# Kernel tuning notes

Hardware: AMD Instinct MI355X
Metric: run time of the kernel (lower is better)

The kernel has to match this reference:

```python
import jax, jax.numpy as jnp
import numpy as np


def _idft_matrix(n):
    # IDFT_n[j,k] = (1/n) * exp(+2*pi*i*j*k/n)  (matches 1/N * DFT**(-1) in source)
    jk = np.outer(np.arange(n), np.arange(n))
    return jnp.asarray((np.exp(2j * np.pi * jk / n) / n).astype(np.complex64))


def setup_inputs() -> dict:
    key = jax.random.key(0)
    B, Y, X = 64, 512, 512
    inp = jax.random.normal(key, (B, Y, X, 2), dtype=jnp.float32)
    return {"inp": inp}


def reference(inp) -> jnp.ndarray:
    B, Y, X, _ = inp.shape
    # pack real/imag channels into complex64
    c = jax.lax.complex(inp[..., 0], inp[..., 1])  # [B, Y, X]
    IDFT_y = _idft_matrix(Y)  # [Y, Y]
    IDFT_x = _idft_matrix(X)  # [X, X]
    # IDFT along Y axis: 'db,abc->adc'
    res1 = jnp.einsum('db,abc->adc', IDFT_y, c)
    # IDFT along X axis then magnitude: 'cd,abc->abd'
    out = jnp.abs(jnp.einsum('cd,abc->abd', IDFT_x, res1))
    return out[..., None]  # [B, Y, X, 1]
```

## Files before the change

kernel.cpp:

```cpp
#include <hip/hip_runtime.h>
#include <math.h>


#define TWO_PI_F 6.283185307179586f

__device__ __forceinline__ float2 cmul(float2 a, float2 b) {
    return make_float2(a.x * b.x - a.y * b.y, a.x * b.y + a.y * b.x);
}
__device__ __forceinline__ float2 cadd(float2 a, float2 b) { return make_float2(a.x + b.x, a.y + b.y); }
__device__ __forceinline__ float2 csub(float2 a, float2 b) { return make_float2(a.x - b.x, a.y - b.y); }
__device__ __forceinline__ float2 csq(float2 a) { return make_float2(a.x * a.x - a.y * a.y, 2.f * a.x * a.y); }
__device__ __forceinline__ unsigned rev9(unsigned v) { return __brev(v) >> 23; }
__device__ __forceinline__ unsigned rev6(unsigned v) { return __brev(v) >> 26; }

__device__ __forceinline__ void fft512(float2* r, float2 A, int l) {
    const float S = 0.70710678118654752f;
    {
        float2 t0 = A;
        float2 t1 = cmul(A, make_float2(S, S));
        float2 t2 = make_float2(-A.y, A.x);
        float2 t3 = cmul(A, make_float2(-S, S));
        float2 u, v;
        u = r[0]; v = r[4]; r[0] = cadd(u, v); r[4] = cmul(csub(u, v), t0);
        u = r[1]; v = r[5]; r[1] = cadd(u, v); r[5] = cmul(csub(u, v), t1);
        u = r[2]; v = r[6]; r[2] = cadd(u, v); r[6] = cmul(csub(u, v), t2);
        u = r[3]; v = r[7]; r[3] = cadd(u, v); r[7] = cmul(csub(u, v), t3);
    }
    float2 A2 = csq(A);
    {
        float2 A2i = make_float2(-A2.y, A2.x);
        float2 u, v;
        u = r[0]; v = r[2]; r[0] = cadd(u, v); r[2] = cmul(csub(u, v), A2);
        u = r[1]; v = r[3]; r[1] = cadd(u, v); r[3] = cmul(csub(u, v), A2i);
        u = r[4]; v = r[6]; r[4] = cadd(u, v); r[6] = cmul(csub(u, v), A2);
        u = r[5]; v = r[7]; r[5] = cadd(u, v); r[7] = cmul(csub(u, v), A2i);
    }
    float2 A4 = csq(A2);
    {
        float2 u, v;
        u = r[0]; v = r[1]; r[0] = cadd(u, v); r[1] = cmul(csub(u, v), A4);
        u = r[2]; v = r[3]; r[2] = cadd(u, v); r[3] = cmul(csub(u, v), A4);
        u = r[4]; v = r[5]; r[4] = cadd(u, v); r[5] = cmul(csub(u, v), A4);
        u = r[6]; v = r[7]; r[6] = cadd(u, v); r[7] = cmul(csub(u, v), A4);
    }
    float2 P = csq(A4);
    #pragma unroll
    for (int mi = 0; mi < 6; ++mi) {
        const int m = 32 >> mi;
        const bool hi = (l & m) != 0;
        #pragma unroll
        for (int k = 0; k < 8; ++k) {
            float2 o;
            o.x = __shfl_xor(r[k].x, m);
            o.y = __shfl_xor(r[k].y, m);
            float2 sum = cadd(r[k], o);
            float2 dif = cmul(csub(r[k], o), P);
            r[k].x = hi ? dif.x : sum.x;
            r[k].y = hi ? dif.y : sum.y;
        }
        if (mi < 5) P = csq(P);
    }
}

__global__ __launch_bounds__(512)
void fft_y_kernel(const float2* __restrict__ in, float2* __restrict__ ws) {
    __shared__ float2 tile[4096];
    const int t = threadIdx.x;
    const int w = t >> 6, l = t & 63;
    const int g = t & 7, q = t >> 3;
    const int x0 = blockIdx.x * 8;
    const int b = blockIdx.y;

    const float2* src = in + ((size_t)b << 18) + x0;
    const int sw = (q & 7) ^ ((q >> 3) & 7);
    #pragma unroll
    for (int it = 0; it < 8; ++it) {
        const int y = it * 64 + q;
        tile[y * 8 + (g ^ sw)] = src[((size_t)y << 9) + g];
    }
    __syncthreads();

    float sA, cA;
    sincosf(TWO_PI_F * (float)l * (1.0f / 512.0f), &sA, &cA);
    float2 r[8];
    const int swl = (l & 7) ^ ((l >> 3) & 7);
    #pragma unroll
    for (int k = 0; k < 8; ++k)
        r[k] = tile[(k * 64 + l) * 8 + (w ^ swl)];

    fft512(r, make_float2(cA, sA), l);

    #pragma unroll
    for (int k = 0; k < 8; ++k)
        tile[(k * 64 + l) * 8 + (w ^ swl)] = r[k];
    __syncthreads();

    float2* dst = ws + ((size_t)b << 18) + x0;
    #pragma unroll
    for (int it = 0; it < 8; ++it) {
        const int y = it * 64 + q;
        dst[((size_t)y << 9) + g] = tile[y * 8 + (g ^ sw)];
    }
}

__global__ __launch_bounds__(256)
void fft_x_mag_kernel(const float2* __restrict__ ws, float* __restrict__ out) {
    const int t = threadIdx.x;
    const int w = t >> 6, l = t & 63;
    const int row = blockIdx.x * 4 + w;
    const int b = row >> 9, ry = row & 511;

    const float2* src = ws + ((size_t)row << 9);
    float2 r[8];
    #pragma unroll
    for (int k = 0; k < 8; ++k)
        r[k] = src[k * 64 + l];

    float sA, cA;
    sincosf(TWO_PI_F * (float)l * (1.0f / 512.0f), &sA, &cA);
    fft512(r, make_float2(cA, sA), l);

    const int rev3k[8] = {0, 4, 2, 6, 1, 5, 3, 7};
    float m[8];
    #pragma unroll
    for (int k = 0; k < 8; ++k) {
        const float2 z = r[k];
        m[rev3k[k]] = sqrtf(z.x * z.x + z.y * z.y) * (1.0f / 262144.0f);
    }

    float* orow = out + (((size_t)(b << 9) + rev9(ry)) << 9);
    const int base = rev6(l) * 8;
    *(float4*)(orow + base)     = make_float4(m[0], m[1], m[2], m[3]);
    *(float4*)(orow + base + 4) = make_float4(m[4], m[5], m[6], m[7]);
}

extern "C" void kernel_launch(void* const* d_in, const int* in_sizes, int n_in,
                              void* d_out, int out_size, void* d_ws, size_t ws_size,
                              hipStream_t stream) {
    const float2* in = (const float2*)d_in[0];
    float2* ws = (float2*)d_ws;
    float* out = (float*)d_out;

    fft_y_kernel<<<dim3(64, 64), 512, 0, stream>>>(in, ws);
    fft_x_mag_kernel<<<8192, 256, 0, stream>>>(ws, out);
}
```

Measured before the change: 294.6 us.

## Store Y-FFT output transposed in natural order; X-FFT reads columns via shared tile

The Y-pass kernel now writes its result directly from registers into a transposed workspace layout ([b][x][y]) with bit-reversal undone per thread. This removes the second shared-memory round trip and the extra barrier. The X-pass kernel switches to tiled loads of 8 columns through swizzled shared memory with float4 global reads, so its output rows come out in natural order and the rev9 row scatter goes away. Global loads are widened to float4 in both kernels. In exchange, both passes now depend on strided-column gathers, and the workspace writes are scattered at 32-byte granularity, which may hurt coalescing.

Result: slower. 303.1 us (+2.9%).

```diff
diff --git a/kernel.cpp b/kernel.cpp
--- a/kernel.cpp
+++ b/kernel.cpp
@@ -10,7 +10,6 @@
 __device__ __forceinline__ float2 cadd(float2 a, float2 b) { return make_float2(a.x + b.x, a.y + b.y); }
 __device__ __forceinline__ float2 csub(float2 a, float2 b) { return make_float2(a.x - b.x, a.y - b.y); }
 __device__ __forceinline__ float2 csq(float2 a) { return make_float2(a.x * a.x - a.y * a.y, 2.f * a.x * a.y); }
-__device__ __forceinline__ unsigned rev9(unsigned v) { return __brev(v) >> 23; }
 __device__ __forceinline__ unsigned rev6(unsigned v) { return __brev(v) >> 26; }
 
 __device__ __forceinline__ void fft512(float2* r, float2 A, int l) {
@@ -63,84 +62,94 @@
 }
 
 __global__ __launch_bounds__(512)
-void fft_y_kernel(const float2* __restrict__ in, float2* __restrict__ ws) {
-    __shared__ float2 tile[4096];
+void fft_y_kernel(const float2* __restrict__ in, float2* __restrict__ wst) {
+    __shared__ float2 tile[8 * 512];
     const int t = threadIdx.x;
     const int w = t >> 6, l = t & 63;
-    const int g = t & 7, q = t >> 3;
+    const int g = t & 3, q = t >> 2;
     const int x0 = blockIdx.x * 8;
-    const int b = blockIdx.y;
+    const int b  = blockIdx.y;
 
     const float2* src = in + ((size_t)b << 18) + x0;
-    const int sw = (q & 7) ^ ((q >> 3) & 7);
     #pragma unroll
-    for (int it = 0; it < 8; ++it) {
-        const int y = it * 64 + q;
-        tile[y * 8 + (g ^ sw)] = src[((size_t)y << 9) + g];
+    for (int it = 0; it < 4; ++it) {
+        const int y = it * 128 + q;
+        const float4 v = *(const float4*)(src + ((size_t)y << 9) + 2 * g);
+        const int ys = y ^ (4 * g);
+        tile[(2 * g) * 512 + ys]     = make_float2(v.x, v.y);
+        tile[(2 * g + 1) * 512 + ys] = make_float2(v.z, v.w);
     }
     __syncthreads();
 
     float sA, cA;
     sincosf(TWO_PI_F * (float)l * (1.0f / 512.0f), &sA, &cA);
     float2 r[8];
-    const int swl = (l & 7) ^ ((l >> 3) & 7);
+    const int sw = 4 * (w >> 1);
     #pragma unroll
     for (int k = 0; k < 8; ++k)
-        r[k] = tile[(k * 64 + l) * 8 + (w ^ swl)];
+        r[k] = tile[w * 512 + ((k * 64 + l) ^ sw)];
 
     fft512(r, make_float2(cA, sA), l);
 
-    #pragma unroll
-    for (int k = 0; k < 8; ++k)
-        tile[(k * 64 + l) * 8 + (w ^ swl)] = r[k];
-    __syncthreads();
-
-    float2* dst = ws + ((size_t)b << 18) + x0;
-    #pragma unroll
-    for (int it = 0; it < 8; ++it) {
-        const int y = it * 64 + q;
-        dst[((size_t)y << 9) + g] = tile[y * 8 + (g ^ sw)];
-    }
+    float2* dst = wst + (((size_t)(b * 512 + x0 + w)) << 9) + rev6((unsigned)l) * 8;
+    *(float4*)(dst + 0) = make_float4(r[0].x, r[0].y, r[4].x, r[4].y);
+    *(float4*)(dst + 2) = make_float4(r[2].x, r[2].y, r[6].x, r[6].y);
+    *(float4*)(dst + 4) = make_float4(r[1].x, r[1].y, r[5].x, r[5].y);
+    *(float4*)(dst + 6) = make_float4(r[3].x, r[3].y, r[7].x, r[7].y);
 }
 
-__global__ __launch_bounds__(256)
-void fft_x_mag_kernel(const float2* __restrict__ ws, float* __restrict__ out) {
+__global__ __launch_bounds__(512)
+void fft_x_mag_kernel(const float2* __restrict__ wst, float* __restrict__ out) {
+    __shared__ float2 tile[8 * 512];
     const int t = threadIdx.x;
     const int w = t >> 6, l = t & 63;
-    const int row = blockIdx.x * 4 + w;
-    const int b = row >> 9, ry = row & 511;
+    const int g = t & 3, q = t >> 2;
+    const int f0 = blockIdx.x * 8;
+    const int b  = blockIdx.y;
 
-    const float2* src = ws + ((size_t)row << 9);
-    float2 r[8];
+    const float2* src = wst + ((size_t)b << 18) + f0;
     #pragma unroll
-    for (int k = 0; k < 8; ++k)
-        r[k] = src[k * 64 + l];
+    for (int it = 0; it < 4; ++it) {
+        const int x = it * 128 + q;
+        const float4 v = *(const float4*)(src + ((size_t)x << 9) + 2 * g);
+        const int xs = x ^ (4 * g);
+        tile[(2 * g) * 512 + xs]     = make_float2(v.x, v.y);
+        tile[(2 * g + 1) * 512 + xs] = make_float2(v.z, v.w);
+    }
+    __syncthreads();
 
     float sA, cA;
     sincosf(TWO_PI_F * (float)l * (1.0f / 512.0f), &sA, &cA);
+    float2 r[8];
+    const int sw = 4 * (w >> 1);
+    #pragma unroll
+    for (int k = 0; k < 8; ++k)
+        r[k] = tile[w * 512 + ((k * 64 + l) ^ sw)];
+
     fft512(r, make_float2(cA, sA), l);
 
-    const int rev3k[8] = {0, 4, 2, 6, 1, 5, 3, 7};
-    float m[8];
-    #pragma unroll
-    for (int k = 0; k < 8; ++k) {
-        const float2 z = r[k];
-        m[rev3k[k]] = sqrtf(z.x * z.x + z.y * z.y) * (1.0f / 262144.0f);
-    }
+    const float s = 1.0f / 262144.0f;
+    float m0 = sqrtf(r[0].x * r[0].x + r[0].y * r[0].y) * s;
+    float m1 = sqrtf(r[4].x * r[4].x + r[4].y * r[4].y) * s;
+    float m2 = sqrtf(r[2].x * r[2].x + r[2].y * r[2].y) * s;
+    float m3 = sqrtf(r[6].x * r[6].x + r[6].y * r[6].y) * s;
+    float m4 = sqrtf(r[1].x * r[1].x + r[1].y * r[1].y) * s;
+    float m5 = sqrtf(r[5].x * r[5].x + r[5].y * r[5].y) * s;
+    float m6 = sqrtf(r[3].x * r[3].x + r[3].y * r[3].y) * s;
+    float m7 = sqrtf(r[7].x * r[7].x + r[7].y * r[7].y) * s;
 
-    float* orow = out + (((size_t)(b << 9) + rev9(ry)) << 9);
-    const int base = rev6(l) * 8;
-    *(float4*)(orow + base)     = make_float4(m[0], m[1], m[2], m[3]);
-    *(float4*)(orow + base + 4) = make_float4(m[4], m[5], m[6], m[7]);
+    float* orow = out + (((size_t)(b * 512 + f0 + w)) << 9) + rev6((unsigned)l) * 8;
+    *(float4*)(orow + 0) = make_float4(m0, m1, m2, m3);
+    *(float4*)(orow + 4) = make_float4(m4, m5, m6, m7);
 }
 
 extern "C" void kernel_launch(void* const* d_in, const int* in_sizes, int n_in,
                               void* d_out, int out_size, void* d_ws, size_t ws_size,
                               hipStream_t stream) {
     const float2* in = (const float2*)d_in[0];
-    float2* ws = (float2*)d_ws;
+    float2* wst = (float2*)d_ws;
     float* out = (float*)d_out;
 
-    fft_y_kernel<<<dim3(64, 64), 512, 0, stream>>>(in, ws);
-    fft_x_mag_kernel<<<8192, 256, 0, stream>>>(ws, out);
+    fft_y_kernel<<<dim3(64, 64), 512, 0, stream>>>(in, wst);
+    fft_x_mag_kernel<<<dim3(64, 64), 512, 0, stream>>>(wst, out);
 }
```
